# Kernel tuning notes

Measured on AMD Instinct MI355X. Metric: run time of the kernel, lower is better.

The kernel has to match this reference:

```python
import jax, jax.numpy as jnp
import numpy as np

B, T, C, H, DH, L, V = 16, 1023, 384, 6, 64, 6, 256
FF = 4 * C
EPS = 1e-5


def _ln(x, g, b):
    mu = x.mean(-1, keepdims=True)
    var = ((x - mu) ** 2).mean(-1, keepdims=True)
    return (x - mu) * jax.lax.rsqrt(var + EPS) * g + b


def setup_inputs() -> dict:
    key = jax.random.key(0)
    ks = jax.random.split(key, 12)
    n = lambda k, shp: jax.random.normal(k, shp, dtype=jnp.float32) * 0.02
    return {
        "x": jax.random.randint(ks[0], (B, T), 0, V),
        "targets": jax.random.randint(ks[1], (B, T), 0, V),
        "tok_emb": n(ks[2], (V, C)),
        "pos_emb": n(ks[3], (T, C)),
        "Wq": n(ks[4], (L, C, C)), "Wk": n(ks[5], (L, C, C)), "Wv": n(ks[6], (L, C, C)),
        "Wo": n(ks[7], (L, C, C)), "bo": jnp.zeros((L, C)),
        "ln1_g": jnp.ones((L, C)), "ln1_b": jnp.zeros((L, C)),
        "ln2_g": jnp.ones((L, C)), "ln2_b": jnp.zeros((L, C)),
        "W1": n(ks[8], (L, C, FF)), "b1": jnp.zeros((L, FF)),
        "W2": n(ks[9], (L, FF, C)), "b2": jnp.zeros((L, C)),
        "lnf_g": jnp.ones((C,)), "lnf_b": jnp.zeros((C,)),
        "Wf": n(ks[10], (C, V)), "bf": jnp.zeros((V,)),
    }


def _forward(x, targets, tok_emb, pos_emb, Wq, Wk, Wv, Wo, bo,
             ln1_g, ln1_b, ln2_g, ln2_b, W1, b1, W2, b2, lnf_g, lnf_b, Wf, bf):
    h = tok_emb[x] + pos_emb[None, :, :]  # [B,T,C]
    tril = jnp.tril(jnp.ones((T, T), bool))

    def heads(z, W):  # [B,T,C] @ [C,C] -> [B,H,T,DH]
        return jnp.einsum('btc,cd->btd', z, W).reshape(B, T, H, DH).transpose(0, 2, 1, 3)

    def layer(h, p):
        wq, wk, wv, wo, bo_, g1, be1, g2, be2, w1, bb1, w2, bb2 = p
        z = _ln(h, g1, be1)
        q, k, v = heads(z, wq), heads(z, wk), heads(z, wv)
        qk = jnp.einsum('bhtd,bhsd->bhts', q, k) * (DH ** -0.5)
        zm = jnp.where(tril, qk, 0.0)
        # faithful to torch: masked_fill_(zeromask == 0, -inf)
        zm = jnp.where(zm == 0.0, -jnp.inf, zm)
        att = jax.nn.softmax(zm, axis=-1)  # dropout = identity (eval)
        o = jnp.einsum('bhts,bhsd->bhtd', att, v).transpose(0, 2, 1, 3).reshape(B, T, C)
        h = h + jnp.einsum('btc,cd->btd', o, wo) + bo_
        z2 = _ln(h, g2, be2)
        ff = jax.nn.relu(jnp.einsum('btc,cf->btf', z2, w1) + bb1)
        h = h + jnp.einsum('btf,fc->btc', ff, w2) + bb2
        return h, None

    params = (Wq, Wk, Wv, Wo, bo, ln1_g, ln1_b, ln2_g, ln2_b, W1, b1, W2, b2)
    h, _ = jax.lax.scan(layer, h, params)
    logits = jnp.einsum('btc,cv->btv', _ln(h, lnf_g, lnf_b), Wf) + bf
    logits2 = logits.reshape(B * T, V)
    logp = jax.nn.log_softmax(logits2, axis=-1)
    loss = -jnp.take_along_axis(logp, targets.reshape(B * T, 1), axis=1).mean()
    return logits2, loss


def reference(x, targets, tok_emb, pos_emb, Wq, Wk, Wv, Wo, bo,
              ln1_g, ln1_b, ln2_g, ln2_b, W1, b1, W2, b2, lnf_g, lnf_b, Wf, bf):
    return _forward(x, targets, tok_emb, pos_emb, Wq, Wk, Wv, Wo, bo,
                    ln1_g, ln1_b, ln2_g, ln2_b, W1, b1, W2, b2, lnf_g, lnf_b, Wf, bf)
```

## Files before the change

kernel.cpp:

```cpp
#include <hip/hip_runtime.h>
#include <hip/hip_bf16.h>
#include <math.h>

#define B_  16
#define T_  1023
#define C_  384
#define H_  6
#define DH_ 64
#define L_  6
#define V_  256
#define FF_ 1536
#define M_  (B_*T_)
#define MP_ 16384
#define EPS_ 1e-5f

typedef __attribute__((ext_vector_type(8))) short bf16x8;
typedef __attribute__((ext_vector_type(4))) short short4v;
typedef __attribute__((ext_vector_type(4))) float f32x4;

__device__ inline short f2bf(float x) {
    union { float f; unsigned u; } c; c.f = x;
    unsigned r = (c.u + 0x7fffu + ((c.u >> 16) & 1u)) >> 16;
    return (short)r;
}

#define GLDS16(g, l) __builtin_amdgcn_global_load_lds(                         \
    (const __attribute__((address_space(1))) void*)(g),                        \
    (__attribute__((address_space(3))) void*)(l), 16, 0, 0)

#define TRRD(dst, va, IMM) asm volatile("ds_read_b64_tr_b16 %0, %1 offset:" IMM \
    : "=v"(dst) : "v"(va))

__global__ void embed_kernel(const int* __restrict__ x, const float* __restrict__ tok,
                             const float* __restrict__ pos, float* __restrict__ h) {
    int i = blockIdx.x * 256 + threadIdx.x;
    if (i >= M_ * C_) return;
    int bt = i / C_;
    int c  = i - bt * C_;
    int t  = bt % T_;
    h[i] = tok[x[bt] * C_ + c] + pos[t * C_ + c];
}

__global__ __launch_bounds__(256) void wconv_kernel(
    const float* __restrict__ Wq, const float* __restrict__ Wk,
    const float* __restrict__ Wv, const float* __restrict__ Wo,
    const float* __restrict__ W1, const float* __restrict__ W2,
    const float* __restrict__ Wf,
    short* __restrict__ qkvt, short* __restrict__ wot, short* __restrict__ w1t,
    short* __restrict__ w2t, short* __restrict__ wft) {
    __shared__ float tile[32][33];
    int t = blockIdx.x;
    const float* src; short* dst; int K, N, tl;
    if (t < 10368) {
        int l = t / 1728, r = t - l * 1728;
        if (r < 432) {
            int which = r / 144; tl = r - which * 144;
            src = (which == 0 ? Wq : which == 1 ? Wk : Wv) + (size_t)l * 384 * 384;
            dst = qkvt + (size_t)l * 1152 * 384 + (size_t)which * 384 * 384;
            K = 384; N = 384;
        } else if (r < 576) {
            tl = r - 432;
            src = Wo + (size_t)l * 384 * 384; dst = wot + (size_t)l * 384 * 384;
            K = 384; N = 384;
        } else if (r < 1152) {
            tl = r - 576;
            src = W1 + (size_t)l * 384 * 1536; dst = w1t + (size_t)l * 1536 * 384;
            K = 384; N = 1536;
        } else {
            tl = r - 1152;
            src = W2 + (size_t)l * 1536 * 384; dst = w2t + (size_t)l * 384 * 1536;
            K = 1536; N = 384;
        }
    } else {
        tl = t - 10368; src = Wf; dst = wft; K = 384; N = 256;
    }
    int ntx = N >> 5;
    int k0 = (tl / ntx) << 5, n0 = (tl % ntx) << 5;
    int rr = threadIdx.x >> 5, cc = threadIdx.x & 31;
#pragma unroll
    for (int p = 0; p < 4; ++p)
        tile[rr + 8 * p][cc] = src[(size_t)(k0 + rr + 8 * p) * N + n0 + cc];
    __syncthreads();
#pragma unroll
    for (int p = 0; p < 4; ++p)
        dst[(size_t)(n0 + rr + 8 * p) * K + k0 + cc] = f2bf(tile[cc][rr + 8 * p]);
}

__global__ __launch_bounds__(256) void ln_kernel(const float* __restrict__ in,
                                                 const float* __restrict__ g,
                                                 const float* __restrict__ b,
                                                 short* __restrict__ out) {
    int wave = threadIdx.x >> 6, lane = threadIdx.x & 63;
    int row  = blockIdx.x * 4 + wave;
    const float* rp = in + (size_t)row * C_;
    float v[6];
    float s = 0.f, s2 = 0.f;
#pragma unroll
    for (int i = 0; i < 6; ++i) {
        v[i] = rp[i * 64 + lane];
        s  += v[i];
        s2 += v[i] * v[i];
    }
#pragma unroll
    for (int o = 32; o > 0; o >>= 1) {
        s  += __shfl_xor(s,  o, 64);
        s2 += __shfl_xor(s2, o, 64);
    }
    float mu  = s * (1.0f / C_);
    float var = s2 * (1.0f / C_) - mu * mu;
    float rs  = rsqrtf(var + EPS_);
    short* op = out + (size_t)row * C_;
#pragma unroll
    for (int i = 0; i < 6; ++i) {
        int c = i * 64 + lane;
        op[c] = f2bf((v[i] - mu) * rs * g[c] + b[c]);
    }
}

template<int MODE, bool RELU, bool HB>
__global__ __launch_bounds__(256) void mm_kernel(const short* __restrict__ A,
                                                 const short* __restrict__ Bt,
                                                 const float* __restrict__ bias,
                                                 short* __restrict__ outb,
                                                 float* __restrict__ outf,
                                                 int N, int K) {
    __shared__ short Al[2][8][128][8];
    __shared__ short Bl[2][8][128][8];
    int tid  = threadIdx.x;
    int wave = tid >> 6, lane = tid & 63;
    int kg4 = lane >> 4, r16 = lane & 15;
    int wr = (wave >> 1) * 64, wc = (wave & 1) * 64;
    int row0 = blockIdx.x * 128, col0 = blockIdx.y * 128;

    const short* ga = A  + (size_t)(row0 + (tid & 127)) * K + ((tid >> 7) << 5);
    const short* gb = Bt + (size_t)(col0 + (tid & 127)) * K + ((tid >> 7) << 5);
    short* alds = &Al[0][0][0][0];
    short* blds = &Bl[0][0][0][0];
    int ldst = ((tid >> 7) << 2) * 1024 + (tid & 127) * 8;

    f32x4 acc[4][4];
#pragma unroll
    for (int i = 0; i < 4; ++i)
#pragma unroll
        for (int j = 0; j < 4; ++j) { acc[i][j][0]=0.f; acc[i][j][1]=0.f; acc[i][j][2]=0.f; acc[i][j][3]=0.f; }

#define MM_STAGE(BUF)                                                          \
    {                                                                          \
        short* la = alds + (BUF) * 8192 + ldst;                                \
        short* lb = blds + (BUF) * 8192 + ldst;                                \
        GLDS16(ga,      la);        GLDS16(ga + 8,  la + 1024);                \
        GLDS16(ga + 16, la + 2048); GLDS16(ga + 24, la + 3072);                \
        GLDS16(gb,      lb);        GLDS16(gb + 8,  lb + 1024);                \
        GLDS16(gb + 16, lb + 2048); GLDS16(gb + 24, lb + 3072);                \
        ga += 64; gb += 64;                                                    \
    }

#define MM_COMPUTE(BUF)                                                        \
    {                                                                          \
        _Pragma("unroll")                                                      \
        for (int p = 0; p < 2; ++p) {                                          \
            const short* ab = alds + (BUF) * 8192 + (4 * p + kg4) * 1024;      \
            const short* bb = blds + (BUF) * 8192 + (4 * p + kg4) * 1024;      \
            bf16x8 av[4], bv[4];                                               \
            _Pragma("unroll")                                                  \
            for (int i = 0; i < 4; ++i) av[i] = *(const bf16x8*)(ab + (wr + 16*i + r16) * 8); \
            _Pragma("unroll")                                                  \
            for (int j = 0; j < 4; ++j) bv[j] = *(const bf16x8*)(bb + (wc + 16*j + r16) * 8); \
            _Pragma("unroll")                                                  \
            for (int i = 0; i < 4; ++i)                                        \
                _Pragma("unroll")                                              \
                for (int j = 0; j < 4; ++j)                                    \
                    acc[i][j] = __builtin_amdgcn_mfma_f32_16x16x32_bf16(av[i], bv[j], acc[i][j], 0, 0, 0); \
        }                                                                      \
    }

    int NT = K >> 6;
    MM_STAGE(0);
    MM_STAGE(1);
    asm volatile("s_waitcnt vmcnt(8)" ::: "memory");
    __builtin_amdgcn_s_barrier();
    asm volatile("" ::: "memory");

    for (int t = 0; t < NT - 1; ++t) {
        MM_COMPUTE(t & 1);
        __builtin_amdgcn_s_barrier();
        asm volatile("" ::: "memory");
        if (t + 2 < NT) {
            MM_STAGE(t & 1);
            asm volatile("s_waitcnt vmcnt(8)" ::: "memory");
        } else {
            asm volatile("s_waitcnt vmcnt(0)" ::: "memory");
        }
        __builtin_amdgcn_s_barrier();
        asm volatile("" ::: "memory");
    }
    MM_COMPUTE((NT - 1) & 1);
#undef MM_STAGE
#undef MM_COMPUTE

#pragma unroll
    for (int j = 0; j < 4; ++j) {
        int col = col0 + wc + 16 * j + r16;
        float bj = HB ? bias[col] : 0.f;
#pragma unroll
        for (int i = 0; i < 4; ++i) {
#pragma unroll
            for (int rg = 0; rg < 4; ++rg) {
                int row = row0 + wr + 16 * i + 4 * kg4 + rg;
                float v = acc[i][j][rg] + bj;
                if (RELU) v = fmaxf(v, 0.f);
                if (MODE == 0) {
                    outb[(size_t)row * N + col] = f2bf(v);
                } else if (MODE == 1) {
                    outf[(size_t)row * N + col] += v;
                } else {
                    if (row < M_) outf[(size_t)row * N + col] = v;
                }
            }
        }
    }
}

__global__ __launch_bounds__(512) void qkv_kernel(const short* __restrict__ z,
                                                  const short* __restrict__ wt,
                                                  short* __restrict__ outb) {
    __shared__ short Zl[48 * 64 * 8];
    int tid  = threadIdx.x;
    int wave = tid >> 6, lane = tid & 63;
    int g = lane >> 4, r16 = lane & 15;
    int r0 = blockIdx.x * 64;

    {
        const short* gz = z + (size_t)(r0 + lane) * C_ + wave * 8;
        short* lz = Zl + (wave * 64 + lane) * 8;
#pragma unroll
        for (int ro = 0; ro < 6; ++ro) { GLDS16(gz, lz); gz += 64; lz += 4096; }
    }

    const short* wbase = wt + (size_t)(16 * wave + r16) * C_ + 8 * g;
    bf16x8 wf[12];
#pragma unroll
    for (int ks = 0; ks < 12; ++ks) wf[ks] = *(const bf16x8*)(wbase + ks * 32);

    asm volatile("s_waitcnt vmcnt(0)" ::: "memory");
    __builtin_amdgcn_s_barrier();
    asm volatile("" ::: "memory");

    for (int c = 0; c < 9; ++c) {
        f32x4 acc[4];
#pragma unroll
        for (int mj = 0; mj < 4; ++mj) { acc[mj][0]=0.f; acc[mj][1]=0.f; acc[mj][2]=0.f; acc[mj][3]=0.f; }
#pragma unroll
        for (int ks = 0; ks < 12; ++ks) {
#pragma unroll
            for (int mj = 0; mj < 4; ++mj) {
                bf16x8 bz = *(const bf16x8*)(Zl + ((4 * ks + g) * 64 + 16 * mj + r16) * 8);
                acc[mj] = __builtin_amdgcn_mfma_f32_16x16x32_bf16(wf[ks], bz, acc[mj], 0, 0, 0);
            }
        }
        if (c + 1 < 9) {
#pragma unroll
            for (int ks = 0; ks < 12; ++ks)
                wf[ks] = *(const bf16x8*)(wbase + (size_t)(c + 1) * 128 * C_ + ks * 32);
        }
#pragma unroll
        for (int mj = 0; mj < 4; ++mj) {
            short4v ov;
#pragma unroll
            for (int rg = 0; rg < 4; ++rg) ov[rg] = f2bf(acc[mj][rg]);
            *(short4v*)(outb + (size_t)(r0 + 16 * mj + r16) * 1152
                        + 128 * c + 16 * wave + 4 * g) = ov;
        }
    }
}

__global__ __launch_bounds__(512) void wo_kernel(const short* __restrict__ ob,
                                                 const short* __restrict__ wt,
                                                 const float* __restrict__ bo,
                                                 float* __restrict__ h,
                                                 const float* __restrict__ lng,
                                                 const float* __restrict__ lnb,
                                                 short* __restrict__ zout) {
    __shared__ short Ol[48 * 64 * 8];
    int tid  = threadIdx.x;
    int wave = tid >> 6, lane = tid & 63;
    int g = lane >> 4, r16 = lane & 15;
    int r0 = blockIdx.x * 64;

    {
        const short* go = ob + (size_t)(r0 + lane) * C_ + wave * 8;
        short* lo = Ol + (wave * 64 + lane) * 8;
#pragma unroll
        for (int ro = 0; ro < 6; ++ro) { GLDS16(go, lo); go += 64; lo += 4096; }
    }

    const short* wbase = wt + (size_t)(48 * wave + r16) * C_ + 8 * g;
    bf16x8 wf[12];
#pragma unroll
    for (int ks2 = 0; ks2 < 4; ++ks2)
#pragma unroll
        for (int j = 0; j < 3; ++j)
            wf[ks2 * 3 + j] = *(const bf16x8*)(wbase + (size_t)(16 * j) * C_ + 32 * ks2);

    asm volatile("s_waitcnt vmcnt(0)" ::: "memory");
    __builtin_amdgcn_s_barrier();
    asm volatile("" ::: "memory");

    f32x4 acc[4][3];
#pragma unroll
    for (int mi = 0; mi < 4; ++mi)
#pragma unroll
        for (int j = 0; j < 3; ++j) { acc[mi][j][0]=0.f; acc[mi][j][1]=0.f; acc[mi][j][2]=0.f; acc[mi][j][3]=0.f; }

    for (int kc = 0; kc < 3; ++kc) {
#pragma unroll
        for (int ks2 = 0; ks2 < 4; ++ks2) {
            bf16x8 pa[4];
#pragma unroll
            for (int mi = 0; mi < 4; ++mi)
                pa[mi] = *(const bf16x8*)(Ol + ((16 * kc + 4 * ks2 + g) * 64 + 16 * mi + r16) * 8);
#pragma unroll
            for (int j = 0; j < 3; ++j)
#pragma unroll
                for (int mi = 0; mi < 4; ++mi)
                    acc[mi][j] = __builtin_amdgcn_mfma_f32_16x16x32_bf16(pa[mi], wf[ks2 * 3 + j], acc[mi][j], 0, 0, 0);
        }
        if (kc + 1 < 3) {
#pragma unroll
            for (int ks2 = 0; ks2 < 4; ++ks2)
#pragma unroll
                for (int j = 0; j < 3; ++j)
                    wf[ks2 * 3 + j] = *(const bf16x8*)(wbase + (size_t)(16 * j) * C_
                                                       + 128 * (kc + 1) + 32 * ks2);
        }
    }
    __syncthreads();

    float rsum[4][4], rsq[4][4];
#pragma unroll
    for (int mi = 0; mi < 4; ++mi)
#pragma unroll
        for (int rg = 0; rg < 4; ++rg) { rsum[mi][rg] = 0.f; rsq[mi][rg] = 0.f; }

#pragma unroll
    for (int j = 0; j < 3; ++j) {
        int col = 48 * wave + 16 * j + r16;
        float bj = bo[col];
#pragma unroll
        for (int mi = 0; mi < 4; ++mi) {
#pragma unroll
            for (int rg = 0; rg < 4; ++rg) {
                int row = r0 + 16 * mi + 4 * g + rg;
                float hv = h[(size_t)row * C_ + col] + acc[mi][j][rg] + bj;
                h[(size_t)row * C_ + col] = hv;
                acc[mi][j][rg] = hv;
                rsum[mi][rg] += hv;
                rsq[mi][rg]  += hv * hv;
            }
        }
    }
#pragma unroll
    for (int o = 1; o < 16; o <<= 1) {
#pragma unroll
        for (int mi = 0; mi < 4; ++mi)
#pragma unroll
            for (int rg = 0; rg < 4; ++rg) {
                rsum[mi][rg] += __shfl_xor(rsum[mi][rg], o, 64);
                rsq[mi][rg]  += __shfl_xor(rsq[mi][rg],  o, 64);
            }
    }
    float* St = (float*)Ol;
    if (r16 == 0) {
#pragma unroll
        for (int mi = 0; mi < 4; ++mi)
#pragma unroll
            for (int rg = 0; rg < 4; ++rg) {
                int rr = 16 * mi + 4 * g + rg;
                St[rr * 16 + 2 * wave]     = rsum[mi][rg];
                St[rr * 16 + 2 * wave + 1] = rsq[mi][rg];
            }
    }
    __syncthreads();
    if (tid < 64) {
        float s = 0.f, s2 = 0.f;
#pragma unroll
        for (int w = 0; w < 8; ++w) { s += St[tid * 16 + 2 * w]; s2 += St[tid * 16 + 2 * w + 1]; }
        float mu  = s * (1.0f / C_);
        float var = s2 * (1.0f / C_) - mu * mu;
        St[tid * 16]     = mu;
        St[tid * 16 + 1] = rsqrtf(var + EPS_);
    }
    __syncthreads();
#pragma unroll
    for (int j = 0; j < 3; ++j) {
        int col = 48 * wave + 16 * j + r16;
        float gam = lng[col], bet = lnb[col];
#pragma unroll
        for (int mi = 0; mi < 4; ++mi) {
#pragma unroll
            for (int rg = 0; rg < 4; ++rg) {
                int rr = 16 * mi + 4 * g + rg;
                float mu = St[rr * 16], rs = St[rr * 16 + 1];
                zout[(size_t)(r0 + rr) * C_ + col] = f2bf((acc[mi][j][rg] - mu) * rs * gam + bet);
            }
        }
    }
}

__global__ __launch_bounds__(512) void ffn_kernel(const short* __restrict__ z,
                                                  const short* __restrict__ w1t,
                                                  const short* __restrict__ w2t,
                                                  const float* __restrict__ b1,
                                                  const float* __restrict__ b2,
                                                  float* __restrict__ h) {
    __shared__ short Zl[48 * 64 * 8];
    __shared__ short Pl[16 * 64 * 8];
    int tid  = threadIdx.x;
    int wave = tid >> 6, lane = tid & 63;
    int g = lane >> 4, r16 = lane & 15;
    int r0 = blockIdx.x * 64;

    {
        const short* gz = z + (size_t)(r0 + lane) * C_ + wave * 8;
        short* lz = Zl + (wave * 64 + lane) * 8;
#pragma unroll
        for (int ro = 0; ro < 6; ++ro) {
            GLDS16(gz, lz);
            gz += 64;
            lz += 8 * 64 * 8;
        }
    }

    const short* w1base = w1t + (size_t)(16 * wave + r16) * C_ + 8 * g;
    const short* w2base = w2t + (size_t)(48 * wave + r16) * FF_ + 8 * g;

    bf16x8 w1f[12];
#pragma unroll
    for (int ks = 0; ks < 12; ++ks)
        w1f[ks] = *(const bf16x8*)(w1base + ks * 32);

    asm volatile("s_waitcnt vmcnt(0)" ::: "memory");
    __builtin_amdgcn_s_barrier();
    asm volatile("" ::: "memory");

    f32x4 acc2[4][3];
#pragma unroll
    for (int mi = 0; mi < 4; ++mi)
#pragma unroll
        for (int j = 0; j < 3; ++j) { acc2[mi][j][0]=0.f; acc2[mi][j][1]=0.f; acc2[mi][j][2]=0.f; acc2[mi][j][3]=0.f; }

    for (int c = 0; c < 12; ++c) {
        bf16x8 w2f[12];
#pragma unroll
        for (int ks2 = 0; ks2 < 4; ++ks2)
#pragma unroll
            for (int j = 0; j < 3; ++j)
                w2f[ks2 * 3 + j] = *(const bf16x8*)(w2base + (size_t)(16 * j) * FF_
                                                    + 128 * c + 32 * ks2);

        f32x4 acc1[4];
#pragma unroll
        for (int mj = 0; mj < 4; ++mj) { acc1[mj][0]=0.f; acc1[mj][1]=0.f; acc1[mj][2]=0.f; acc1[mj][3]=0.f; }
#pragma unroll
        for (int ks = 0; ks < 12; ++ks) {
#pragma unroll
            for (int mj = 0; mj < 4; ++mj) {
                bf16x8 bz = *(const bf16x8*)(Zl + ((4 * ks + g) * 64 + 16 * mj + r16) * 8);
                acc1[mj] = __builtin_amdgcn_mfma_f32_16x16x32_bf16(w1f[ks], bz, acc1[mj], 0, 0, 0);
            }
        }
        f32x4 b1v = *(const f32x4*)(b1 + 128 * c + 16 * wave + 4 * g);
        int oct = 2 * wave + (g >> 1);
#pragma unroll
        for (int mj = 0; mj < 4; ++mj) {
            short4v pv;
#pragma unroll
            for (int rg = 0; rg < 4; ++rg)
                pv[rg] = f2bf(fmaxf(acc1[mj][rg] + b1v[rg], 0.f));
            *(short4v*)(Pl + (oct * 64 + 16 * mj + r16) * 8 + (g & 1) * 4) = pv;
        }
        __syncthreads();

        if (c + 1 < 12) {
#pragma unroll
            for (int ks = 0; ks < 12; ++ks)
                w1f[ks] = *(const bf16x8*)(w1base + (size_t)(c + 1) * 128 * C_ + ks * 32);
        }

#pragma unroll
        for (int ks2 = 0; ks2 < 4; ++ks2) {
            bf16x8 pa[4];
#pragma unroll
            for (int mi = 0; mi < 4; ++mi)
                pa[mi] = *(const bf16x8*)(Pl + ((4 * ks2 + g) * 64 + 16 * mi + r16) * 8);
#pragma unroll
            for (int j = 0; j < 3; ++j) {
#pragma unroll
                for (int mi = 0; mi < 4; ++mi)
                    acc2[mi][j] = __builtin_amdgcn_mfma_f32_16x16x32_bf16(pa[mi], w2f[ks2 * 3 + j], acc2[mi][j], 0, 0, 0);
            }
        }
        __syncthreads();
    }

#pragma unroll
    for (int j = 0; j < 3; ++j) {
        int col = 48 * wave + 16 * j + r16;
        float bj = b2[col];
#pragma unroll
        for (int mi = 0; mi < 4; ++mi) {
#pragma unroll
            for (int rg = 0; rg < 4; ++rg) {
                int row = r0 + 16 * mi + 4 * g + rg;
                h[(size_t)row * C_ + col] += acc2[mi][j][rg] + bj;
            }
        }
    }
}

__device__ __forceinline__ void attn_step(int kt, int qg, int g, int r16,
                                          const char* Kb, unsigned ka, unsigned va,
                                          short (*Pw)[40],
                                          bf16x8 qf0, bf16x8 qf1,
                                          f32x4* o_acc, float& m, float& l) {
    f32x4 s0, s1;
    s0[0]=0.f;s0[1]=0.f;s0[2]=0.f;s0[3]=0.f;
    s1[0]=0.f;s1[1]=0.f;s1[2]=0.f;s1[3]=0.f;
    bf16x8 a00 = *(const bf16x8*)(Kb + ka);
    bf16x8 a01 = *(const bf16x8*)(Kb + (ka ^ 64u));
    bf16x8 a10 = *(const bf16x8*)(Kb + ka + 2048u);
    bf16x8 a11 = *(const bf16x8*)(Kb + ((ka + 2048u) ^ 64u));
    s0 = __builtin_amdgcn_mfma_f32_16x16x32_bf16(a00, qf0, s0, 0, 0, 0);
    s0 = __builtin_amdgcn_mfma_f32_16x16x32_bf16(a01, qf1, s0, 0, 0, 0);
    s1 = __builtin_amdgcn_mfma_f32_16x16x32_bf16(a10, qf0, s1, 0, 0, 0);
    s1 = __builtin_amdgcn_mfma_f32_16x16x32_bf16(a11, qf1, s1, 0, 0, 0);

    int kb0 = kt * 32 + 4 * g;
    float sv[8];
#pragma unroll
    for (int r = 0; r < 4; ++r) {
        sv[r]     = (kb0 + r      <= qg) ? s0[r] * 0.125f : -3e38f;
        sv[4 + r] = (kb0 + 16 + r <= qg) ? s1[r] * 0.125f : -3e38f;
    }
    float pmax = sv[0];
#pragma unroll
    for (int i = 1; i < 8; ++i) pmax = fmaxf(pmax, sv[i]);
    pmax = fmaxf(pmax, __shfl_xor(pmax, 16, 64));
    pmax = fmaxf(pmax, __shfl_xor(pmax, 32, 64));
    float mn   = fmaxf(m, pmax);
    float corr = __expf(m - mn);
    float rs = 0.f;
    short pb[8];
#pragma unroll
    for (int i = 0; i < 8; ++i) {
        float p = __expf(sv[i] - mn);
        rs += p;
        pb[i] = f2bf(p);
    }
    rs += __shfl_xor(rs, 16, 64);
    rs += __shfl_xor(rs, 32, 64);
    l = l * corr + rs;
    m = mn;

    short4v t0w, t1w;
    t0w[0]=pb[0]; t0w[1]=pb[1]; t0w[2]=pb[2]; t0w[3]=pb[3];
    t1w[0]=pb[4]; t1w[1]=pb[5]; t1w[2]=pb[6]; t1w[3]=pb[7];
    *(short4v*)&Pw[r16][4 * g]      = t0w;
    *(short4v*)&Pw[r16][16 + 4 * g] = t1w;

    short4v v0, v1, v2, v3, v4, v5, v6, v7;
    TRRD(v0, va, "0");    TRRD(v1, va, "512");
    TRRD(v2, va, "128");  TRRD(v3, va, "640");
    TRRD(v4, va, "256");  TRRD(v5, va, "768");
    TRRD(v6, va, "384");  TRRD(v7, va, "896");

    bf16x8 pB = *(const bf16x8*)&Pw[r16][8 * g];
#pragma unroll
    for (int d = 0; d < 4; ++d) {
        o_acc[d][0] *= corr; o_acc[d][1] *= corr;
        o_acc[d][2] *= corr; o_acc[d][3] *= corr;
    }
    asm volatile("s_waitcnt lgkmcnt(0)" ::: "memory");
    __builtin_amdgcn_sched_barrier(0);

    bf16x8 av0, av1, av2, av3;
#pragma unroll
    for (int i = 0; i < 4; ++i) {
        av0[i] = v0[i]; av0[i + 4] = v1[i];
        av1[i] = v2[i]; av1[i + 4] = v3[i];
        av2[i] = v4[i]; av2[i + 4] = v5[i];
        av3[i] = v6[i]; av3[i + 4] = v7[i];
    }
    o_acc[0] = __builtin_amdgcn_mfma_f32_16x16x32_bf16(av0, pB, o_acc[0], 0, 0, 0);
    o_acc[1] = __builtin_amdgcn_mfma_f32_16x16x32_bf16(av1, pB, o_acc[1], 0, 0, 0);
    o_acc[2] = __builtin_amdgcn_mfma_f32_16x16x32_bf16(av2, pB, o_acc[2], 0, 0, 0);
    o_acc[3] = __builtin_amdgcn_mfma_f32_16x16x32_bf16(av3, pB, o_acc[3], 0, 0, 0);
}

__global__ __launch_bounds__(256) void attn_kernel(const short* __restrict__ qkv,
                                                   short* __restrict__ o) {
    __shared__ short Kl[32 * 64];
    __shared__ short Vl[32 * 64];
    __shared__ short P_lds[4][16][40];

    int tid  = threadIdx.x;
    int wave = tid >> 6;
    int lane = tid & 63;
    int g    = lane >> 4;
    int r16  = lane & 15;

    int qtA = blockIdx.x;
    int qtB = 15 - qtA;
    int bh = blockIdx.y;
    int b  = bh / H_, hh = bh - b * H_;
    size_t rbase = (size_t)b * T_;
    int qoff = hh * 64;

    int q0A = qtA * 64, q0B = qtB * 64;
    int qgA = q0A + wave * 16 + r16;
    int qgB = q0B + wave * 16 + r16;

    const short* qrA = qkv + (rbase + qgA) * 1152 + qoff;
    const short* qrB = qkv + (rbase + qgB) * 1152 + qoff;
    bf16x8 qfA0 = *(const bf16x8*)(qrA + 8 * g);
    bf16x8 qfA1 = *(const bf16x8*)(qrA + 32 + 8 * g);
    bf16x8 qfB0 = *(const bf16x8*)(qrB + 8 * g);
    bf16x8 qfB1 = *(const bf16x8*)(qrB + 32 + 8 * g);

    int kkey = tid >> 3;
    int koct = (tid & 7) ^ (kkey & 7);
    const short* gk = qkv + (rbase + kkey) * 1152 + qoff + 384 + koct * 8;
    int vkey = 4 * (tid >> 5) + ((tid >> 1) & 3);
    int voct = 2 * ((tid >> 3) & 3) + (tid & 1);
    const short* gv = qkv + (rbase + vkey) * 1152 + qoff + 768 + voct * 8;
    short* lk = Kl + tid * 8;
    short* lv = Vl + tid * 8;

    f32x4 oA[4], oB[4];
#pragma unroll
    for (int d = 0; d < 4; ++d) {
        oA[d][0]=0.f; oA[d][1]=0.f; oA[d][2]=0.f; oA[d][3]=0.f;
        oB[d][0]=0.f; oB[d][1]=0.f; oB[d][2]=0.f; oB[d][3]=0.f;
    }
    float mA = -3e38f, lA = 0.f, mB = -3e38f, lB = 0.f;

    const char* Kb = (const char*)Kl;
    unsigned ka = (unsigned)(r16 * 128 + ((g ^ (r16 & 7)) << 4));
    unsigned va = (unsigned)(size_t)(__attribute__((address_space(3))) short*)Vl
                + 1024u * (unsigned)g + 8u * (unsigned)r16;

    int ktA_hi = (q0A + wave * 16 + 15) >> 5;
    int ktB_hi = (q0B + wave * 16 + 15) >> 5;
    int nkt = 2 * (qtB + 1);

    for (int kt = 0; kt < nkt; ++kt) {
        __syncthreads();
        GLDS16(gk, lk);
        GLDS16(gv, lv);
        gk += 32 * 1152; gv += 32 * 1152;
        __syncthreads();

        if (kt <= ktB_hi)
            attn_step(kt, qgB, g, r16, Kb, ka, va, P_lds[wave], qfB0, qfB1, oB, mB, lB);
        if (kt <= ktA_hi)
            attn_step(kt, qgA, g, r16, Kb, ka, va, P_lds[wave], qfA0, qfA1, oA, mA, lA);
    }

    {
        float inv = (lA > 0.f) ? 1.f / lA : 0.f;
        short* orow = o + (rbase + qgA) * C_ + qoff;
#pragma unroll
        for (int d = 0; d < 4; ++d) {
            short4v ov;
#pragma unroll
            for (int r = 0; r < 4; ++r) ov[r] = f2bf(oA[d][r] * inv);
            *(short4v*)(orow + 16 * d + 4 * g) = ov;
        }
    }
    if (qgB < T_) {
        float inv = (lB > 0.f) ? 1.f / lB : 0.f;
        short* orow = o + (rbase + qgB) * C_ + qoff;
#pragma unroll
        for (int d = 0; d < 4; ++d) {
            short4v ov;
#pragma unroll
            for (int r = 0; r < 4; ++r) ov[r] = f2bf(oB[d][r] * inv);
            *(short4v*)(orow + 16 * d + 4 * g) = ov;
        }
    }
}

__global__ __launch_bounds__(256) void nll_kernel(const float* __restrict__ logits,
                                                  const int* __restrict__ tgt,
                                                  float* __restrict__ nll) {
    int wave = threadIdx.x >> 6, lane = threadIdx.x & 63;
    int row  = blockIdx.x * 4 + wave;
    const float* rp = logits + (size_t)row * V_;
    float v[4];
    float mx = -INFINITY;
#pragma unroll
    for (int i = 0; i < 4; ++i) {
        v[i] = rp[i * 64 + lane];
        mx = fmaxf(mx, v[i]);
    }
#pragma unroll
    for (int o = 32; o > 0; o >>= 1) mx = fmaxf(mx, __shfl_xor(mx, o, 64));
    float s = 0.f;
#pragma unroll
    for (int i = 0; i < 4; ++i) s += expf(v[i] - mx);
#pragma unroll
    for (int o = 32; o > 0; o >>= 1) s += __shfl_xor(s, o, 64);
    if (lane == 0) {
        float lse = mx + logf(s);
        nll[row] = lse - rp[tgt[row]];
    }
}

__global__ __launch_bounds__(256) void loss_kernel(const float* __restrict__ nll,
                                                   float* __restrict__ loss) {
    __shared__ float sm[256];
    float s = 0.f;
    for (int i = threadIdx.x; i < M_; i += 256) s += nll[i];
    sm[threadIdx.x] = s;
    __syncthreads();
    for (int o = 128; o > 0; o >>= 1) {
        if (threadIdx.x < o) sm[threadIdx.x] += sm[threadIdx.x + o];
        __syncthreads();
    }
    if (threadIdx.x == 0) *loss = sm[0] * (1.0f / M_);
}

extern "C" void kernel_launch(void* const* d_in, const int* in_sizes, int n_in,
                              void* d_out, int out_size, void* d_ws, size_t ws_size,
                              hipStream_t stream) {
    const int*   x       = (const int*)d_in[0];
    const int*   targets = (const int*)d_in[1];
    const float* tok_emb = (const float*)d_in[2];
    const float* pos_emb = (const float*)d_in[3];
    const float* Wq      = (const float*)d_in[4];
    const float* Wk      = (const float*)d_in[5];
    const float* Wv      = (const float*)d_in[6];
    const float* Wo      = (const float*)d_in[7];
    const float* bo      = (const float*)d_in[8];
    const float* ln1_g   = (const float*)d_in[9];
    const float* ln1_b   = (const float*)d_in[10];
    const float* ln2_g   = (const float*)d_in[11];
    const float* ln2_b   = (const float*)d_in[12];
    const float* W1      = (const float*)d_in[13];
    const float* b1      = (const float*)d_in[14];
    const float* W2      = (const float*)d_in[15];
    const float* b2      = (const float*)d_in[16];
    const float* lnf_g   = (const float*)d_in[17];
    const float* lnf_b   = (const float*)d_in[18];
    const float* Wf      = (const float*)d_in[19];
    const float* bf      = (const float*)d_in[20];

    float* logits = (float*)d_out;
    float* loss   = logits + (size_t)M_ * V_;

    float* h    = (float*)d_ws;
    short* z    = (short*)(h + (size_t)MP_ * C_);
    short* big  = z + (size_t)MP_ * C_;
    short* ob   = big + (size_t)MP_ * FF_;
    short* qkvt = ob + (size_t)MP_ * C_;
    short* wot  = qkvt + (size_t)L_ * 1152 * 384;
    short* w1t  = wot + (size_t)L_ * 384 * 384;
    short* w2t  = w1t + (size_t)L_ * 1536 * 384;
    short* wft  = w2t + (size_t)L_ * 1536 * 384;
    float* nll  = (float*)(wft + (size_t)256 * 384);

    wconv_kernel<<<10464, 256, 0, stream>>>(Wq, Wk, Wv, Wo, W1, W2, Wf,
                                            qkvt, wot, w1t, w2t, wft);
    embed_kernel<<<(M_ * C_ + 255) / 256, 256, 0, stream>>>(x, tok_emb, pos_emb, h);

    for (int l = 0; l < L_; ++l) {
        ln_kernel<<<M_ / 4, 256, 0, stream>>>(h, ln1_g + l * C_, ln1_b + l * C_, z);
        qkv_kernel<<<MP_ / 64, 512, 0, stream>>>(z, qkvt + (size_t)l * 1152 * 384, big);
        attn_kernel<<<dim3(8, B_ * H_), 256, 0, stream>>>(big, ob);
        wo_kernel<<<MP_ / 64, 512, 0, stream>>>(
            ob, wot + (size_t)l * 384 * 384, bo + l * C_, h,
            ln2_g + l * C_, ln2_b + l * C_, z);
        ffn_kernel<<<MP_ / 64, 512, 0, stream>>>(
            z, w1t + (size_t)l * 1536 * 384, w2t + (size_t)l * 384 * 1536,
            b1 + l * FF_, b2 + l * C_, h);
    }

    ln_kernel<<<M_ / 4, 256, 0, stream>>>(h, lnf_g, lnf_b, z);
    mm_kernel<2, false, true><<<dim3(128, 2), 256, 0, stream>>>(
        z, wft, bf, nullptr, logits, 256, 384);

    nll_kernel<<<M_ / 4, 256, 0, stream>>>(logits, targets, nll);
    loss_kernel<<<1, 256, 0, stream>>>(nll, loss);
}
```

Measured before the change: 1.275 ms.

## Double-buffer K/V tiles in attention kernel to overlap loads with compute

Splits the K and V shared-memory tiles into two buffers and prefetches the next key tile with direct global-to-LDS loads while the current tile is processed. The two barriers per iteration become one barrier preceded by a vmcnt wait at the end of each step. This aims to hide global load latency behind the MFMA and softmax work. It doubles the K/V LDS footprint, which could lower occupancy.

```diff
diff --git a/kernel.cpp b/kernel.cpp
--- a/kernel.cpp
+++ b/kernel.cpp
@@ -599,8 +599,8 @@
 
 __global__ __launch_bounds__(256) void attn_kernel(const short* __restrict__ qkv,
                                                    short* __restrict__ o) {
-    __shared__ short Kl[32 * 64];
-    __shared__ short Vl[32 * 64];
+    __shared__ short Kl[2][32 * 64];
+    __shared__ short Vl[2][32 * 64];
     __shared__ short P_lds[4][16][40];
 
     int tid  = threadIdx.x;
@@ -633,8 +633,10 @@
     int vkey = 4 * (tid >> 5) + ((tid >> 1) & 3);
     int voct = 2 * ((tid >> 3) & 3) + (tid & 1);
     const short* gv = qkv + (rbase + vkey) * 1152 + qoff + 768 + voct * 8;
-    short* lk = Kl + tid * 8;
-    short* lv = Vl + tid * 8;
+    short* lk0 = Kl[0] + tid * 8;
+    short* lk1 = Kl[1] + tid * 8;
+    short* lv0 = Vl[0] + tid * 8;
+    short* lv1 = Vl[1] + tid * 8;
 
     f32x4 oA[4], oB[4];
 #pragma unroll
@@ -644,26 +646,42 @@
     }
     float mA = -3e38f, lA = 0.f, mB = -3e38f, lB = 0.f;
 
-    const char* Kb = (const char*)Kl;
+    const char* Kb0 = (const char*)Kl[0];
+    const char* Kb1 = (const char*)Kl[1];
     unsigned ka = (unsigned)(r16 * 128 + ((g ^ (r16 & 7)) << 4));
-    unsigned va = (unsigned)(size_t)(__attribute__((address_space(3))) short*)Vl
-                + 1024u * (unsigned)g + 8u * (unsigned)r16;
+    unsigned va0 = (unsigned)(size_t)(__attribute__((address_space(3))) short*)Vl[0]
+                 + 1024u * (unsigned)g + 8u * (unsigned)r16;
+    unsigned va1 = va0 + 4096u;
 
     int ktA_hi = (q0A + wave * 16 + 15) >> 5;
     int ktB_hi = (q0B + wave * 16 + 15) >> 5;
     int nkt = 2 * (qtB + 1);
 
+    GLDS16(gk, lk0);
+    GLDS16(gv, lv0);
+    gk += 32 * 1152; gv += 32 * 1152;
+    asm volatile("s_waitcnt vmcnt(0)" ::: "memory");
+    __builtin_amdgcn_s_barrier();
+    asm volatile("" ::: "memory");
+
     for (int kt = 0; kt < nkt; ++kt) {
-        __syncthreads();
-        GLDS16(gk, lk);
-        GLDS16(gv, lv);
-        gk += 32 * 1152; gv += 32 * 1152;
-        __syncthreads();
+        int cur = kt & 1;
+        if (kt + 1 < nkt) {
+            GLDS16(gk, cur ? lk0 : lk1);
+            GLDS16(gv, cur ? lv0 : lv1);
+            gk += 32 * 1152; gv += 32 * 1152;
+        }
+        const char* Kb = cur ? Kb1 : Kb0;
+        unsigned va = cur ? va1 : va0;
 
         if (kt <= ktB_hi)
             attn_step(kt, qgB, g, r16, Kb, ka, va, P_lds[wave], qfB0, qfB1, oB, mB, lB);
         if (kt <= ktA_hi)
             attn_step(kt, qgA, g, r16, Kb, ka, va, P_lds[wave], qfA0, qfA1, oA, mA, lA);
+
+        asm volatile("s_waitcnt vmcnt(0)" ::: "memory");
+        __builtin_amdgcn_s_barrier();
+        asm volatile("" ::: "memory");
     }
 
     {
```

Measured after the change: 1.254 ms. No clear change (-1.7%).
